# Kernel tuning notes

Hardware: AMD Instinct MI355X
Metric: run time of the kernel (lower is better)

The kernel has to match this reference:

```python
import jax, jax.numpy as jnp
import numpy as np

D_MODEL, NHEAD, DIM_FF = 256, 8, 2048
B, Q, HW = 8, 100, 128 * 128
EPS = 1e-5


def _layernorm(x, g, b):
    mu = jnp.mean(x, axis=-1, keepdims=True)
    var = jnp.mean(jnp.square(x - mu), axis=-1, keepdims=True)
    return (x - mu) * jax.lax.rsqrt(var + EPS) * g + b


def _mha(x_q, x_kv, in_w, in_b, out_w, out_b, nhead, mask=None):
    """torch.nn.MultiheadAttention (batch_first). mask: (B*H,Q,S) bool, True=ATTEND."""
    d = x_q.shape[-1]
    wq, wk, wv = jnp.split(in_w, 3, axis=0)
    bq, bk, bv = jnp.split(in_b, 3)
    q = x_q @ wq.T + bq          # (B,Q,d)
    k = x_kv @ wk.T + bk         # (B,S,d)
    v = x_kv @ wv.T + bv
    Bb, Qq, _ = q.shape
    S = k.shape[1]
    hd = d // nhead
    q = q.reshape(Bb, Qq, nhead, hd).transpose(0, 2, 1, 3)   # (B,H,Q,hd)
    k = k.reshape(Bb, S, nhead, hd).transpose(0, 2, 1, 3)    # (B,H,S,hd)
    v = v.reshape(Bb, S, nhead, hd).transpose(0, 2, 1, 3)
    scores = jnp.einsum('bhqd,bhkd->bhqk', q, k) / jnp.sqrt(jnp.asarray(hd, q.dtype))
    if mask is not None:
        m = mask.reshape(Bb, nhead, Qq, S)
        scores = jnp.where(m, scores, -jnp.inf)
    attn = jax.nn.softmax(scores, axis=-1)
    out = jnp.einsum('bhqk,bhkd->bhqd', attn, v)             # (B,H,Q,hd)
    out = out.transpose(0, 2, 1, 3).reshape(Bb, Qq, d)
    return out @ out_w.T + out_b


def setup_inputs() -> dict:
    key = jax.random.key(0)
    ks = jax.random.split(key, 10)
    s = 0.02
    return {
        'queries': jax.random.normal(ks[0], (B, Q, D_MODEL), jnp.float32),
        'pixel_features': jax.random.normal(ks[1], (B, HW, D_MODEL), jnp.float32),
        'attn_mask': jax.random.randint(ks[2], (B * NHEAD, Q, HW), 0, 2).astype(bool),
        'sa_in_w': jax.random.normal(ks[3], (3 * D_MODEL, D_MODEL), jnp.float32) * s,
        'sa_in_b': jnp.zeros((3 * D_MODEL,), jnp.float32),
        'sa_out_w': jax.random.normal(ks[4], (D_MODEL, D_MODEL), jnp.float32) * s,
        'sa_out_b': jnp.zeros((D_MODEL,), jnp.float32),
        'norm1_g': jnp.ones((D_MODEL,), jnp.float32),
        'norm1_b': jnp.zeros((D_MODEL,), jnp.float32),
        'ca_in_w': jax.random.normal(ks[5], (3 * D_MODEL, D_MODEL), jnp.float32) * s,
        'ca_in_b': jnp.zeros((3 * D_MODEL,), jnp.float32),
        'ca_out_w': jax.random.normal(ks[6], (D_MODEL, D_MODEL), jnp.float32) * s,
        'ca_out_b': jnp.zeros((D_MODEL,), jnp.float32),
        'norm2_g': jnp.ones((D_MODEL,), jnp.float32),
        'norm2_b': jnp.zeros((D_MODEL,), jnp.float32),
        'ff_w1': jax.random.normal(ks[7], (DIM_FF, D_MODEL), jnp.float32) * s,
        'ff_b1': jnp.zeros((DIM_FF,), jnp.float32),
        'ff_w2': jax.random.normal(ks[8], (D_MODEL, DIM_FF), jnp.float32) * s,
        'ff_b2': jnp.zeros((D_MODEL,), jnp.float32),
        'norm3_g': jnp.ones((D_MODEL,), jnp.float32),
        'norm3_b': jnp.zeros((D_MODEL,), jnp.float32),
    }


def reference(queries, pixel_features, attn_mask,
              sa_in_w, sa_in_b, sa_out_w, sa_out_b, norm1_g, norm1_b,
              ca_in_w, ca_in_b, ca_out_w, ca_out_b, norm2_g, norm2_b,
              ff_w1, ff_b1, ff_w2, ff_b2, norm3_g, norm3_b):
    # 1) self-attention among queries (post-norm residual)
    sa = _mha(queries, queries, sa_in_w, sa_in_b, sa_out_w, sa_out_b, NHEAD)
    x = _layernorm(queries + sa, norm1_g, norm1_b)
    # 2) masked cross-attention (attn_mask: True = attend)
    ca = _mha(x, pixel_features, ca_in_w, ca_in_b, ca_out_w, ca_out_b, NHEAD, mask=attn_mask)
    x = _layernorm(x + ca, norm2_g, norm2_b)
    # 3) FFN
    h = jax.nn.relu(x @ ff_w1.T + ff_b1)
    ff = h @ ff_w2.T + ff_b2
    return _layernorm(x + ff, norm3_g, norm3_b)
```

## Files before the change

kernel.cpp:

```cpp
#include <hip/hip_runtime.h>

#define SCALE 0.17677669529663687f

typedef __attribute__((ext_vector_type(8))) short frag8;
typedef __attribute__((ext_vector_type(4))) float facc4;

#define MFMA16(a, b, c) __builtin_amdgcn_mfma_f32_16x16x32_bf16((a), (b), (c), 0, 0, 0)

__device__ __forceinline__ unsigned short f2b(float f) {
  union { float f; unsigned u; } v; v.f = f;
  return (unsigned short)((v.u + 0x7fffu + ((v.u >> 16) & 1u)) >> 16);
}
__device__ __forceinline__ unsigned int pack2(float a, float b) {
  return (unsigned int)f2b(a) | ((unsigned int)f2b(b) << 16);
}
__device__ __forceinline__ void gl_lds16(const void* g, void* l) {
  __builtin_amdgcn_global_load_lds((const __attribute__((address_space(1))) unsigned int*)g,
                                   (__attribute__((address_space(3))) unsigned int*)l, 16, 0, 0);
}

__global__ __launch_bounds__(256) void cvt_weights(const float* __restrict__ s0, const float* __restrict__ s1,
                                                   const float* __restrict__ s2, const float* __restrict__ s3,
                                                   const float* __restrict__ s4, const float* __restrict__ s5,
                                                   unsigned short* __restrict__ dst) {
  int bid = blockIdx.x;
  const float* src; int off;
  if (bid < 96)       { src = s0; off = 0; }
  else if (bid < 128) { src = s1; off = 196608; bid -= 96; }
  else if (bid < 224) { src = s2; off = 262144; bid -= 128; }
  else if (bid < 256) { src = s3; off = 458752; bid -= 224; }
  else if (bid < 512) { src = s4; off = 524288; bid -= 256; }
  else                { src = s5; off = 1048576; bid -= 512; }
  int i = bid * 2048 + threadIdx.x * 8;
  float4 a = *(const float4*)(src + i);
  float4 b = *(const float4*)(src + i + 4);
  uint4 p;
  p.x = pack2(a.x, a.y); p.y = pack2(a.z, a.w);
  p.z = pack2(b.x, b.y); p.w = pack2(b.z, b.w);
  *(uint4*)(dst + off + i) = p;
}

__global__ __launch_bounds__(256) void pack_mask(const unsigned char* __restrict__ mask,
                                                 unsigned int* __restrict__ mp) {
  int idx = blockIdx.x * 256 + threadIdx.x;
  if (idx >= 64 * 112 * 512) return;
  int wi = idx & 511;
  int row = (idx >> 9) % 112;
  int bh = idx / (512 * 112);
  unsigned int wv = 0;
  if (row < 100) {
    const unsigned int* src = (const unsigned int*)(mask + (size_t)(bh * 100 + row) * 16384 + wi * 32);
#pragma unroll
    for (int u = 0; u < 8; ++u) {
      unsigned int nib = (((src[u] & 0x01010101u) * 0x01020408u) >> 24) & 0xFu;
      wv |= nib << (u * 4);
    }
  }
  mp[idx] = wv;
}

template <int RELU, int BIAS>
__global__ __launch_bounds__(256) void mfma_gemm(const float* __restrict__ A,
                                                 const unsigned short* __restrict__ Wb,
                                                 const float* __restrict__ bias,
                                                 float* __restrict__ C,
                                                 int M, int N, int Ktot, int Kchunk) {
  __shared__ unsigned short As[64 * 40];
  __shared__ unsigned short Bs[64 * 32];
  const int t = threadIdx.x;
  const int mb = blockIdx.x, nb = blockIdx.y, zb = blockIdx.z;
  const int w = t >> 6, lane = t & 63, quad = lane >> 4, l16 = lane & 15;
  const int kbeg = zb * Kchunk;
  float* Cz = C + (size_t)zb * M * N;
  facc4 acc[4] = {};
  for (int k0 = kbeg; k0 < kbeg + Kchunk; k0 += 32) {
    {
      int r = t >> 2, c = (t & 3) * 8;
      int gr = mb * 64 + r;
      float4 f0 = {}, f1 = {};
      if (gr < M) {
        const float* src = A + (size_t)gr * Ktot + k0 + c;
        f0 = *(const float4*)src; f1 = *(const float4*)(src + 4);
      }
      uint4 p;
      p.x = pack2(f0.x, f0.y); p.y = pack2(f0.z, f0.w);
      p.z = pack2(f1.x, f1.y); p.w = pack2(f1.z, f1.w);
      *(uint4*)&As[r * 40 + c] = p;
    }
    {
      int row = w * 16 + (lane >> 2);
      gl_lds16(Wb + (size_t)(nb * 64 + row) * Ktot + k0 + (lane & 3) * 8, Bs + w * 512);
    }
    __syncthreads();
    frag8 af = *(const frag8*)(As + (w * 16 + l16) * 40 + quad * 8);
#pragma unroll
    for (int nt = 0; nt < 4; ++nt) {
      frag8 bf = *(const frag8*)(Bs + (nt * 16 + l16) * 32 + quad * 8);
      acc[nt] = MFMA16(af, bf, acc[nt]);
    }
    __syncthreads();
  }
#pragma unroll
  for (int nt = 0; nt < 4; ++nt)
#pragma unroll
    for (int rg = 0; rg < 4; ++rg) {
      int row = mb * 64 + w * 16 + quad * 4 + rg;
      int col = nb * 64 + nt * 16 + l16;
      if (row < M) {
        float v = acc[nt][rg] + (BIAS ? bias[col] : 0.f);
        if (RELU) v = fmaxf(v, 0.f);
        Cz[(size_t)row * N + col] = v;
      }
    }
}

__global__ __launch_bounds__(256) void res_ln(const float* __restrict__ y,
                                              const float* __restrict__ resid,
                                              const float* __restrict__ g,
                                              const float* __restrict__ bv,
                                              float* __restrict__ out) {
  const int r = blockIdx.x, t = threadIdx.x;
  float v = y[(size_t)r * 256 + t] + resid[(size_t)r * 256 + t];
  __shared__ float red[8];
  float s1 = v, s2 = v * v;
#pragma unroll
  for (int off = 1; off < 64; off <<= 1) { s1 += __shfl_xor(s1, off, 64); s2 += __shfl_xor(s2, off, 64); }
  if ((t & 63) == 0) { red[t >> 6] = s1; red[4 + (t >> 6)] = s2; }
  __syncthreads();
  float S1 = red[0] + red[1] + red[2] + red[3];
  float S2 = red[4] + red[5] + red[6] + red[7];
  float mu = S1 * (1.f / 256.f);
  float var = S2 * (1.f / 256.f) - mu * mu;
  float inv = rsqrtf(var + 1e-5f);
  out[(size_t)r * 256 + t] = (v - mu) * inv * g[t] + bv[t];
}

__global__ __launch_bounds__(256) void res_ln4(const float* __restrict__ p,
                                               const float* __restrict__ bias,
                                               const float* __restrict__ resid,
                                               const float* __restrict__ g,
                                               const float* __restrict__ bv,
                                               float* __restrict__ out) {
  const int r = blockIdx.x, t = threadIdx.x;
  size_t i = (size_t)r * 256 + t;
  float v = p[i] + p[i + 204800] + p[i + 409600] + p[i + 614400] + bias[t] + resid[i];
  __shared__ float red[8];
  float s1 = v, s2 = v * v;
#pragma unroll
  for (int off = 1; off < 64; off <<= 1) { s1 += __shfl_xor(s1, off, 64); s2 += __shfl_xor(s2, off, 64); }
  if ((t & 63) == 0) { red[t >> 6] = s1; red[4 + (t >> 6)] = s2; }
  __syncthreads();
  float S1 = red[0] + red[1] + red[2] + red[3];
  float S2 = red[4] + red[5] + red[6] + red[7];
  float mu = S1 * (1.f / 256.f);
  float var = S2 * (1.f / 256.f) - mu * mu;
  float inv = rsqrtf(var + 1e-5f);
  out[i] = (v - mu) * inv * g[t] + bv[t];
}

__global__ __launch_bounds__(256) void self_attn(const float* __restrict__ qkv,
                                                 float* __restrict__ out) {
  const int wid = blockIdx.x * 4 + (threadIdx.x >> 6);
  const int lane = threadIdx.x & 63;
  const int bh = wid / 100, q = wid - bh * 100;
  const int b = bh >> 3, h = bh & 7;
  float4 qv[8];
  {
    const float4* qr = (const float4*)(qkv + (size_t)(b * 100 + q) * 768 + h * 32);
#pragma unroll
    for (int i = 0; i < 8; ++i) {
      float4 x = qr[i];
      qv[i] = make_float4(x.x * SCALE, x.y * SCALE, x.z * SCALE, x.w * SCALE);
    }
  }
  float l = 0.f;
  float4 O[8] = {};
  for (int k0 = 0; k0 < 128; k0 += 64) {
    int k = k0 + lane;
    int kc = (k < 100) ? k : 0;
    const float4* kr = (const float4*)(qkv + (size_t)(b * 100 + kc) * 768 + 256 + h * 32);
    float s = 0.f;
#pragma unroll
    for (int i = 0; i < 8; ++i) {
      float4 kx = kr[i];
      s += qv[i].x * kx.x + qv[i].y * kx.y + qv[i].z * kx.z + qv[i].w * kx.w;
    }
    float p = (k < 100) ? __expf(s) : 0.f;
    l += p;
    const float4* vr = (const float4*)(qkv + (size_t)(b * 100 + kc) * 768 + 512 + h * 32);
#pragma unroll
    for (int i = 0; i < 8; ++i) {
      float4 vx = vr[i];
      O[i].x += p * vx.x; O[i].y += p * vx.y; O[i].z += p * vx.z; O[i].w += p * vx.w;
    }
  }
#pragma unroll
  for (int off = 1; off < 64; off <<= 1) {
    l += __shfl_xor(l, off, 64);
#pragma unroll
    for (int i = 0; i < 8; ++i) {
      O[i].x += __shfl_xor(O[i].x, off, 64);
      O[i].y += __shfl_xor(O[i].y, off, 64);
      O[i].z += __shfl_xor(O[i].z, off, 64);
      O[i].w += __shfl_xor(O[i].w, off, 64);
    }
  }
  if (lane < 32) {
    float inv = 1.f / l;
    int i4 = lane >> 2, sub = lane & 3;
    float ov = 0.f;
#pragma unroll
    for (int i = 0; i < 8; ++i) {
      if (i4 == i) {
        float4 vv = O[i];
        ov = (sub == 0) ? vv.x : (sub == 1) ? vv.y : (sub == 2) ? vv.z : vv.w;
      }
    }
    out[(size_t)(b * 100 + q) * 256 + h * 32 + lane] = ov * inv;
  }
}

__global__ __launch_bounds__(512) void kv_proj(const float* __restrict__ pix,
                                               const unsigned short* __restrict__ wkv,
                                               const float* __restrict__ bkv,
                                               unsigned short* __restrict__ Kbuf,
                                               unsigned short* __restrict__ Vt) {
  __shared__ unsigned short smem[2560 + 16384];
  unsigned short* As = smem;
  unsigned short* Bs = smem + 2560;
  const int t = threadIdx.x;
  const int mb = blockIdx.x;
  const int w = t >> 6, lane = t & 63, quad = lane >> 4, l16 = lane & 15;
  const int b = mb >> 8;
  const int hw0 = (mb & 255) * 64;

  facc4 acc[4][4] = {};
  for (int k0 = 0; k0 < 256; k0 += 32) {
    {
      int r = t >> 3, c = (t & 7) * 4;
      float4 f = *(const float4*)(pix + (size_t)(mb * 64 + r) * 256 + k0 + c);
      uint2 p; p.x = pack2(f.x, f.y); p.y = pack2(f.z, f.w);
      *(uint2*)&As[r * 40 + c] = p;
    }
    {
#pragma unroll
      for (int i = 0; i < 4; ++i) {
        int seg = w * 4 + i;
        int row = seg * 16 + (lane >> 2);
        gl_lds16(wkv + (size_t)row * 256 + k0 + (lane & 3) * 8, Bs + seg * 512);
      }
    }
    __syncthreads();
    frag8 af[4], bf[4];
#pragma unroll
    for (int mt = 0; mt < 4; ++mt) af[mt] = *(const frag8*)(As + (mt * 16 + l16) * 40 + quad * 8);
#pragma unroll
    for (int nt = 0; nt < 4; ++nt) bf[nt] = *(const frag8*)(Bs + (w * 64 + nt * 16 + l16) * 32 + quad * 8);
#pragma unroll
    for (int mt = 0; mt < 4; ++mt)
#pragma unroll
      for (int nt = 0; nt < 4; ++nt) acc[mt][nt] = MFMA16(af[mt], bf[nt], acc[mt][nt]);
    __syncthreads();
  }
  {
    unsigned short* Cs = smem;
    if (w < 4) {
#pragma unroll
      for (int mt = 0; mt < 4; ++mt)
#pragma unroll
        for (int nt = 0; nt < 4; ++nt) {
          int col = w * 64 + nt * 16 + l16;
          float bvv = bkv[col];
#pragma unroll
          for (int rg = 0; rg < 4; ++rg)
            Cs[(mt * 16 + quad * 4 + rg) * 264 + col] = f2b(acc[mt][nt][rg] + bvv);
        }
    }
    __syncthreads();
    int key = t >> 3, h = t & 7;
    const unsigned short* src = &Cs[key * 264 + h * 32];
    unsigned short* dst = Kbuf + ((size_t)((b * 8 + h) * 16384 + hw0 + key)) * 32;
    uint4 c0 = *(const uint4*)src, c1 = *(const uint4*)(src + 8);
    uint4 c2 = *(const uint4*)(src + 16), c3 = *(const uint4*)(src + 24);
    *(uint4*)dst = c0; *(uint4*)(dst + 8) = c1; *(uint4*)(dst + 16) = c2; *(uint4*)(dst + 24) = c3;
  }
  __syncthreads();
  {
    unsigned short* Cst = smem;
    if (w >= 4) {
#pragma unroll
      for (int mt = 0; mt < 4; ++mt)
#pragma unroll
        for (int nt = 0; nt < 4; ++nt) {
          int colv = (w - 4) * 64 + nt * 16 + l16;
          float bvv = bkv[256 + colv];
#pragma unroll
          for (int rg = 0; rg < 4; ++rg)
            Cst[colv * 72 + (mt * 16 + quad * 4 + rg)] = f2b(acc[mt][nt][rg] + bvv);
        }
    }
    __syncthreads();
    int dr = t >> 1, half = t & 1;
    const unsigned short* src = &Cst[dr * 72 + half * 32];
    unsigned short* dst = Vt + ((size_t)(b * 8 + (dr >> 5)) * 32 + (dr & 31)) * 16384 + hw0 + half * 32;
    uint4 c0 = *(const uint4*)src, c1 = *(const uint4*)(src + 8);
    uint4 c2 = *(const uint4*)(src + 16), c3 = *(const uint4*)(src + 24);
    *(uint4*)dst = c0; *(uint4*)(dst + 8) = c1; *(uint4*)(dst + 16) = c2; *(uint4*)(dst + 24) = c3;
  }
}

__global__ __launch_bounds__(256) void cross_attn(const float* __restrict__ qc,
                                                  const unsigned short* __restrict__ Kbuf,
                                                  const unsigned short* __restrict__ Vt,
                                                  const unsigned int* __restrict__ maskp,
                                                  float* __restrict__ Opart,
                                                  float* __restrict__ lpart) {
  const int bh = blockIdx.x >> 3;
  const int chunk = blockIdx.x & 7;
  const int b = bh >> 3, h = bh & 7;
  const int t = threadIdx.x;
  const int w = t >> 6, lane = t & 63, quad = lane >> 4, l16 = lane & 15;

  __shared__ unsigned short Qs[112 * 40];
  for (int i = t; i < 112 * 32; i += 256) {
    int r = i >> 5, d = i & 31;
    float v = (r < 100) ? qc[(size_t)(b * 100 + r) * 256 + h * 32 + d] * SCALE : 0.f;
    Qs[r * 40 + d] = f2b(v);
  }
  __syncthreads();

  frag8 qf[7];
#pragma unroll
  for (int qt = 0; qt < 7; ++qt) qf[qt] = *(const frag8*)(Qs + (qt * 16 + l16) * 40 + quad * 8);

  facc4 o[7][2] = {};
  float lacc[7] = {};
  const facc4 zacc = {0.f, 0.f, 0.f, 0.f};
  const int keybase = chunk * 2048 + w * 512;
  const unsigned short* Kb = Kbuf + (size_t)bh * 16384 * 32;
  const unsigned short* Vb = Vt + (size_t)bh * 32 * 16384;
  const unsigned int* mrow = maskp + (size_t)bh * 112 * 512;

  for (int it = 0; it < 16; ++it) {
    const int kk = keybase + it * 32;
    frag8 kf0 = *(const frag8*)(Kb + (size_t)(kk + l16) * 32 + quad * 8);
    frag8 kf1 = *(const frag8*)(Kb + (size_t)(kk + 16 + l16) * 32 + quad * 8);
    frag8 vf[2];
#pragma unroll
    for (int dt = 0; dt < 2; ++dt) {
      const unsigned short* vp = Vb + (size_t)(dt * 16 + l16) * 16384 + kk + quad * 4;
      ushort4 lo = *(const ushort4*)vp;
      ushort4 hi = *(const ushort4*)(vp + 16);
      frag8 v;
      v[0] = (short)lo.x; v[1] = (short)lo.y; v[2] = (short)lo.z; v[3] = (short)lo.w;
      v[4] = (short)hi.x; v[5] = (short)hi.y; v[6] = (short)hi.z; v[7] = (short)hi.w;
      vf[dt] = v;
    }
    const int wi = kk >> 5;
#pragma unroll
    for (int qt = 0; qt < 7; ++qt) {
      facc4 s0 = MFMA16(kf0, qf[qt], zacc);
      facc4 s1 = MFMA16(kf1, qf[qt], zacc);
      unsigned int mw = mrow[(qt * 16 + l16) * 512 + wi];
      float p[8];
#pragma unroll
      for (int rg = 0; rg < 4; ++rg) {
        float e0 = __expf(s0[rg]);
        float e1 = __expf(s1[rg]);
        p[rg]     = ((mw >> (quad * 4 + rg)) & 1u) ? e0 : 0.f;
        p[4 + rg] = ((mw >> (16 + quad * 4 + rg)) & 1u) ? e1 : 0.f;
      }
      lacc[qt] += p[0] + p[1] + p[2] + p[3] + p[4] + p[5] + p[6] + p[7];
      frag8 pa;
#pragma unroll
      for (int j = 0; j < 8; ++j) pa[j] = (short)f2b(p[j]);
      o[qt][0] = MFMA16(pa, vf[0], o[qt][0]);
      o[qt][1] = MFMA16(pa, vf[1], o[qt][1]);
    }
  }
#pragma unroll
  for (int qt = 0; qt < 7; ++qt) {
    lacc[qt] += __shfl_xor(lacc[qt], 16, 64);
    lacc[qt] += __shfl_xor(lacc[qt], 32, 64);
  }
  const int pidx = chunk * 4 + w;
  float* Op = Opart + ((size_t)bh * 32 + pidx) * 112 * 32;
  float* lp = lpart + ((size_t)bh * 32 + pidx) * 112;
#pragma unroll
  for (int qt = 0; qt < 7; ++qt) {
#pragma unroll
    for (int rg = 0; rg < 4; ++rg) {
      int row = qt * 16 + quad * 4 + rg;
      Op[row * 32 + l16] = o[qt][0][rg];
      Op[row * 32 + 16 + l16] = o[qt][1][rg];
    }
    if (lane < 16) lp[qt * 16 + lane] = lacc[qt];
  }
}

__global__ __launch_bounds__(256) void cross_combine(const float* __restrict__ Opart,
                                                     const float* __restrict__ lpart,
                                                     float* __restrict__ out) {
  const int bid = blockIdx.x;
  const int bh = bid / 13, qg = bid - bh * 13;
  const int t = threadIdx.x;
  const int q = qg * 8 + (t >> 5), d = t & 31;
  if (q >= 100) return;
  const int b = bh >> 3, h = bh & 7;
  float osum = 0.f, lsum = 0.f;
#pragma unroll 4
  for (int p = 0; p < 32; ++p) {
    osum += Opart[(((size_t)bh * 32 + p) * 112 + q) * 32 + d];
    lsum += lpart[((size_t)bh * 32 + p) * 112 + q];
  }
  out[(size_t)(b * 100 + q) * 256 + h * 32 + d] = osum / lsum;
}

extern "C" void kernel_launch(void* const* d_in, const int* in_sizes, int n_in,
                              void* d_out, int out_size, void* d_ws, size_t ws_size,
                              hipStream_t stream) {
  const float* queries = (const float*)d_in[0];
  const float* pix = (const float*)d_in[1];
  const unsigned char* mask = (const unsigned char*)d_in[2];
  const float* sa_in_w = (const float*)d_in[3];
  const float* sa_in_b = (const float*)d_in[4];
  const float* sa_out_w = (const float*)d_in[5];
  const float* sa_out_b = (const float*)d_in[6];
  const float* n1g = (const float*)d_in[7];
  const float* n1b = (const float*)d_in[8];
  const float* ca_in_w = (const float*)d_in[9];
  const float* ca_in_b = (const float*)d_in[10];
  const float* ca_out_w = (const float*)d_in[11];
  const float* ca_out_b = (const float*)d_in[12];
  const float* n2g = (const float*)d_in[13];
  const float* n2b = (const float*)d_in[14];
  const float* ff_w1 = (const float*)d_in[15];
  const float* ff_b1 = (const float*)d_in[16];
  const float* ff_w2 = (const float*)d_in[17];
  const float* ff_b2 = (const float*)d_in[18];
  const float* n3g = (const float*)d_in[19];
  const float* n3b = (const float*)d_in[20];
  float* out = (float*)d_out;
  char* ws = (char*)d_ws;

  unsigned short* Kbuf = (unsigned short*)(ws + 0);
  unsigned short* Vt   = (unsigned short*)(ws + 67108864);
  unsigned short* wb   = (unsigned short*)(ws + 134217728);
  unsigned int* maskp  = (unsigned int*)(ws + 137363456);
  float* qkvs   = (float*)(ws + 152043520);
  float* sao    = (float*)(ws + 154501120);
  float* ptmp   = (float*)(ws + 155320320);
  float* x1     = (float*)(ws + 158597120);
  float* qc     = (float*)(ws + 159416320);
  float* Opart  = (float*)(ws + 160235520);
  float* lpart  = (float*)(ws + 189595648);
  float* ca_out = (float*)(ws + 190513152);
  float* x2     = (float*)(ws + 191332352);
  float* hffn   = (float*)(ws + 192151552);

  const unsigned short* wb_sain  = wb;
  const unsigned short* wb_saout = wb + 196608;
  const unsigned short* wb_caq   = wb + 262144;
  const unsigned short* wb_cakv  = wb + 327680;
  const unsigned short* wb_caout = wb + 458752;
  const unsigned short* wb_ff1   = wb + 524288;
  const unsigned short* wb_ff2   = wb + 1048576;

  cvt_weights<<<768, 256, 0, stream>>>(sa_in_w, sa_out_w, ca_in_w, ca_out_w, ff_w1, ff_w2, wb);
  pack_mask<<<14336, 256, 0, stream>>>(mask, maskp);

  mfma_gemm<0, 1><<<dim3(13, 12, 1), 256, 0, stream>>>(queries, wb_sain, sa_in_b, qkvs, 800, 768, 256, 256);
  self_attn<<<1600, 256, 0, stream>>>(qkvs, sao);
  mfma_gemm<0, 1><<<dim3(13, 4, 1), 256, 0, stream>>>(sao, wb_saout, sa_out_b, ptmp, 800, 256, 256, 256);
  res_ln<<<800, 256, 0, stream>>>(ptmp, queries, n1g, n1b, x1);

  mfma_gemm<0, 1><<<dim3(13, 4, 1), 256, 0, stream>>>(x1, wb_caq, ca_in_b, qc, 800, 256, 256, 256);
  kv_proj<<<2048, 512, 0, stream>>>(pix, wb_cakv, ca_in_b + 256, Kbuf, Vt);
  cross_attn<<<512, 256, 0, stream>>>(qc, Kbuf, Vt, maskp, Opart, lpart);
  cross_combine<<<64 * 13, 256, 0, stream>>>(Opart, lpart, ca_out);
  mfma_gemm<0, 1><<<dim3(13, 4, 1), 256, 0, stream>>>(ca_out, wb_caout, ca_out_b, ptmp, 800, 256, 256, 256);
  res_ln<<<800, 256, 0, stream>>>(ptmp, x1, n2g, n2b, x2);

  mfma_gemm<1, 1><<<dim3(13, 32, 1), 256, 0, stream>>>(x2, wb_ff1, ff_b1, hffn, 800, 2048, 256, 256);
  mfma_gemm<0, 0><<<dim3(13, 4, 4), 256, 0, stream>>>(hffn, wb_ff2, nullptr, ptmp, 800, 256, 2048, 512);
  res_ln4<<<800, 256, 0, stream>>>(ptmp, ff_b2, x2, n3g, n3b, out);
}
```

Measured before the change: 867.1 us.

## Fuse K/V projection, mask packing and cross-attention into one kernel

Replaces the separate kv_proj, pack_mask and cross_attn kernels with a single ca_fused kernel. It projects each 32-key pixel tile to per-head K and V on the fly with MFMA, reads the raw byte mask directly, and uses exp2 with a folded log2e scale. This avoids writing and re-reading 128MB of bf16 K/V and the packed mask. Partial outputs are stored as bf16 and pixels are truncated rather than rounded to bf16. The cost is that every head recomputes projections from a shared pixel tile, weight fragments are reread from global memory in the inner loop, and the grid is only 256 blocks, which may underfill the GPU.

```diff
diff --git a/kernel.cpp b/kernel.cpp
--- a/kernel.cpp
+++ b/kernel.cpp
@@ -1,6 +1,7 @@
 #include <hip/hip_runtime.h>
 
 #define SCALE 0.17677669529663687f
+#define SCALE2 (0.17677669529663687f * 1.4426950408889634f)
 
 typedef __attribute__((ext_vector_type(8))) short frag8;
 typedef __attribute__((ext_vector_type(4))) float facc4;
@@ -11,13 +12,23 @@
   union { float f; unsigned u; } v; v.f = f;
   return (unsigned short)((v.u + 0x7fffu + ((v.u >> 16) & 1u)) >> 16);
 }
+__device__ __forceinline__ float b2f(unsigned short h) {
+  union { unsigned u; float f; } v; v.u = ((unsigned)h) << 16;
+  return v.f;
+}
 __device__ __forceinline__ unsigned int pack2(float a, float b) {
   return (unsigned int)f2b(a) | ((unsigned int)f2b(b) << 16);
+}
+__device__ __forceinline__ unsigned int tpack(float a, float b) {
+  union { float f; unsigned u; } x, y; x.f = a; y.f = b;
+  return (x.u >> 16) | (y.u & 0xffff0000u);
 }
 __device__ __forceinline__ void gl_lds16(const void* g, void* l) {
   __builtin_amdgcn_global_load_lds((const __attribute__((address_space(1))) unsigned int*)g,
                                    (__attribute__((address_space(3))) unsigned int*)l, 16, 0, 0);
 }
+
+union F8U { frag8 f; unsigned u[4]; };
 
 __global__ __launch_bounds__(256) void cvt_weights(const float* __restrict__ s0, const float* __restrict__ s1,
                                                    const float* __restrict__ s2, const float* __restrict__ s3,
@@ -38,25 +49,6 @@
   p.x = pack2(a.x, a.y); p.y = pack2(a.z, a.w);
   p.z = pack2(b.x, b.y); p.w = pack2(b.z, b.w);
   *(uint4*)(dst + off + i) = p;
-}
-
-__global__ __launch_bounds__(256) void pack_mask(const unsigned char* __restrict__ mask,
-                                                 unsigned int* __restrict__ mp) {
-  int idx = blockIdx.x * 256 + threadIdx.x;
-  if (idx >= 64 * 112 * 512) return;
-  int wi = idx & 511;
-  int row = (idx >> 9) % 112;
-  int bh = idx / (512 * 112);
-  unsigned int wv = 0;
-  if (row < 100) {
-    const unsigned int* src = (const unsigned int*)(mask + (size_t)(bh * 100 + row) * 16384 + wi * 32);
-#pragma unroll
-    for (int u = 0; u < 8; ++u) {
-      unsigned int nib = (((src[u] & 0x01010101u) * 0x01020408u) >> 24) & 0xFu;
-      wv |= nib << (u * 4);
-    }
-  }
-  mp[idx] = wv;
 }
 
 template <int RELU, int BIAS>
@@ -220,185 +212,152 @@
   }
 }
 
-__global__ __launch_bounds__(512) void kv_proj(const float* __restrict__ pix,
-                                               const unsigned short* __restrict__ wkv,
-                                               const float* __restrict__ bkv,
-                                               unsigned short* __restrict__ Kbuf,
-                                               unsigned short* __restrict__ Vt) {
-  __shared__ unsigned short smem[2560 + 16384];
-  unsigned short* As = smem;
-  unsigned short* Bs = smem + 2560;
+__global__ __launch_bounds__(512, 2) void ca_fused(const float* __restrict__ qc,
+                                                   const unsigned short* __restrict__ wkv,
+                                                   const float* __restrict__ bkv,
+                                                   const float* __restrict__ pix,
+                                                   const unsigned char* __restrict__ mask,
+                                                   unsigned short* __restrict__ Opartb,
+                                                   float* __restrict__ lpart) {
+  const int bid = blockIdx.x;
+  const int b = bid >> 5, chunk = bid & 31;
   const int t = threadIdx.x;
-  const int mb = blockIdx.x;
-  const int w = t >> 6, lane = t & 63, quad = lane >> 4, l16 = lane & 15;
-  const int b = mb >> 8;
-  const int hw0 = (mb & 255) * 64;
-
-  facc4 acc[4][4] = {};
-  for (int k0 = 0; k0 < 256; k0 += 32) {
-    {
-      int r = t >> 3, c = (t & 7) * 4;
-      float4 f = *(const float4*)(pix + (size_t)(mb * 64 + r) * 256 + k0 + c);
-      uint2 p; p.x = pack2(f.x, f.y); p.y = pack2(f.z, f.w);
-      *(uint2*)&As[r * 40 + c] = p;
-    }
-    {
-#pragma unroll
-      for (int i = 0; i < 4; ++i) {
-        int seg = w * 4 + i;
-        int row = seg * 16 + (lane >> 2);
-        gl_lds16(wkv + (size_t)row * 256 + k0 + (lane & 3) * 8, Bs + seg * 512);
-      }
-    }
-    __syncthreads();
-    frag8 af[4], bf[4];
-#pragma unroll
-    for (int mt = 0; mt < 4; ++mt) af[mt] = *(const frag8*)(As + (mt * 16 + l16) * 40 + quad * 8);
-#pragma unroll
-    for (int nt = 0; nt < 4; ++nt) bf[nt] = *(const frag8*)(Bs + (w * 64 + nt * 16 + l16) * 32 + quad * 8);
-#pragma unroll
-    for (int mt = 0; mt < 4; ++mt)
-#pragma unroll
-      for (int nt = 0; nt < 4; ++nt) acc[mt][nt] = MFMA16(af[mt], bf[nt], acc[mt][nt]);
-    __syncthreads();
-  }
-  {
-    unsigned short* Cs = smem;
-    if (w < 4) {
-#pragma unroll
-      for (int mt = 0; mt < 4; ++mt)
-#pragma unroll
-        for (int nt = 0; nt < 4; ++nt) {
-          int col = w * 64 + nt * 16 + l16;
-          float bvv = bkv[col];
-#pragma unroll
-          for (int rg = 0; rg < 4; ++rg)
-            Cs[(mt * 16 + quad * 4 + rg) * 264 + col] = f2b(acc[mt][nt][rg] + bvv);
-        }
-    }
-    __syncthreads();
-    int key = t >> 3, h = t & 7;
-    const unsigned short* src = &Cs[key * 264 + h * 32];
-    unsigned short* dst = Kbuf + ((size_t)((b * 8 + h) * 16384 + hw0 + key)) * 32;
-    uint4 c0 = *(const uint4*)src, c1 = *(const uint4*)(src + 8);
-    uint4 c2 = *(const uint4*)(src + 16), c3 = *(const uint4*)(src + 24);
-    *(uint4*)dst = c0; *(uint4*)(dst + 8) = c1; *(uint4*)(dst + 16) = c2; *(uint4*)(dst + 24) = c3;
-  }
-  __syncthreads();
-  {
-    unsigned short* Cst = smem;
-    if (w >= 4) {
-#pragma unroll
-      for (int mt = 0; mt < 4; ++mt)
-#pragma unroll
-        for (int nt = 0; nt < 4; ++nt) {
-          int colv = (w - 4) * 64 + nt * 16 + l16;
-          float bvv = bkv[256 + colv];
-#pragma unroll
-          for (int rg = 0; rg < 4; ++rg)
-            Cst[colv * 72 + (mt * 16 + quad * 4 + rg)] = f2b(acc[mt][nt][rg] + bvv);
-        }
-    }
-    __syncthreads();
-    int dr = t >> 1, half = t & 1;
-    const unsigned short* src = &Cst[dr * 72 + half * 32];
-    unsigned short* dst = Vt + ((size_t)(b * 8 + (dr >> 5)) * 32 + (dr & 31)) * 16384 + hw0 + half * 32;
-    uint4 c0 = *(const uint4*)src, c1 = *(const uint4*)(src + 8);
-    uint4 c2 = *(const uint4*)(src + 16), c3 = *(const uint4*)(src + 24);
-    *(uint4*)dst = c0; *(uint4*)(dst + 8) = c1; *(uint4*)(dst + 16) = c2; *(uint4*)(dst + 24) = c3;
-  }
-}
-
-__global__ __launch_bounds__(256) void cross_attn(const float* __restrict__ qc,
-                                                  const unsigned short* __restrict__ Kbuf,
-                                                  const unsigned short* __restrict__ Vt,
-                                                  const unsigned int* __restrict__ maskp,
-                                                  float* __restrict__ Opart,
-                                                  float* __restrict__ lpart) {
-  const int bh = blockIdx.x >> 3;
-  const int chunk = blockIdx.x & 7;
-  const int b = bh >> 3, h = bh & 7;
-  const int t = threadIdx.x;
-  const int w = t >> 6, lane = t & 63, quad = lane >> 4, l16 = lane & 15;
-
-  __shared__ unsigned short Qs[112 * 40];
-  for (int i = t; i < 112 * 32; i += 256) {
-    int r = i >> 5, d = i & 31;
-    float v = (r < 100) ? qc[(size_t)(b * 100 + r) * 256 + h * 32 + d] * SCALE : 0.f;
-    Qs[r * 40 + d] = f2b(v);
-  }
-  __syncthreads();
+  const int h = t >> 6, lane = t & 63, quad = lane >> 4, l16 = lane & 15;
+  const int bh = b * 8 + h;
+
+  __shared__ unsigned short PixS[8 * 32 * 40];
 
   frag8 qf[7];
 #pragma unroll
-  for (int qt = 0; qt < 7; ++qt) qf[qt] = *(const frag8*)(Qs + (qt * 16 + l16) * 40 + quad * 8);
+  for (int qt = 0; qt < 7; ++qt) {
+    int r = qt * 16 + l16;
+    float4 f0 = {}, f1 = {};
+    if (r < 100) {
+      const float* qrow = qc + (size_t)(b * 100 + r) * 256 + h * 32 + quad * 4;
+      f0 = *(const float4*)qrow;
+      f1 = *(const float4*)(qrow + 16);
+    }
+    F8U u;
+    u.u[0] = pack2(f0.x * SCALE2, f0.y * SCALE2);
+    u.u[1] = pack2(f0.z * SCALE2, f0.w * SCALE2);
+    u.u[2] = pack2(f1.x * SCALE2, f1.y * SCALE2);
+    u.u[3] = pack2(f1.z * SCALE2, f1.w * SCALE2);
+    qf[qt] = u.f;
+  }
+
+  float bK[2][4], bV[2];
+#pragma unroll
+  for (int mf = 0; mf < 2; ++mf) {
+#pragma unroll
+    for (int rg = 0; rg < 4; ++rg) bK[mf][rg] = bkv[h * 32 + mf * 16 + quad * 4 + rg];
+    bV[mf] = bkv[256 + h * 32 + mf * 16 + l16];
+  }
+
+  const unsigned short* wkbase = wkv + (size_t)(h * 32) * 256;
+  const unsigned short* wvbase = wkv + (size_t)(256 + h * 32) * 256;
 
   facc4 o[7][2] = {};
   float lacc[7] = {};
   const facc4 zacc = {0.f, 0.f, 0.f, 0.f};
-  const int keybase = chunk * 2048 + w * 512;
-  const unsigned short* Kb = Kbuf + (size_t)bh * 16384 * 32;
-  const unsigned short* Vb = Vt + (size_t)bh * 32 * 16384;
-  const unsigned int* mrow = maskp + (size_t)bh * 112 * 512;
 
   for (int it = 0; it < 16; ++it) {
-    const int kk = keybase + it * 32;
-    frag8 kf0 = *(const frag8*)(Kb + (size_t)(kk + l16) * 32 + quad * 8);
-    frag8 kf1 = *(const frag8*)(Kb + (size_t)(kk + 16 + l16) * 32 + quad * 8);
-    frag8 vf[2];
-#pragma unroll
-    for (int dt = 0; dt < 2; ++dt) {
-      const unsigned short* vp = Vb + (size_t)(dt * 16 + l16) * 16384 + kk + quad * 4;
-      ushort4 lo = *(const ushort4*)vp;
-      ushort4 hi = *(const ushort4*)(vp + 16);
-      frag8 v;
-      v[0] = (short)lo.x; v[1] = (short)lo.y; v[2] = (short)lo.z; v[3] = (short)lo.w;
-      v[4] = (short)hi.x; v[5] = (short)hi.y; v[6] = (short)hi.z; v[7] = (short)hi.w;
-      vf[dt] = v;
-    }
-    const int wi = kk >> 5;
+    const int kk = it * 32;
+    const int gkey = chunk * 512 + kk;
+    __syncthreads();
+    {
+      int row = t >> 4, cg = (t & 15) * 16;
+      const float* src = pix + ((size_t)(b * 16384 + gkey + row)) * 256 + cg;
+      float4 a0 = *(const float4*)src;
+      float4 a1 = *(const float4*)(src + 4);
+      float4 a2 = *(const float4*)(src + 8);
+      float4 a3 = *(const float4*)(src + 12);
+      uint4 u0, u1;
+      u0.x = tpack(a0.x, a0.y); u0.y = tpack(a0.z, a0.w);
+      u0.z = tpack(a1.x, a1.y); u0.w = tpack(a1.z, a1.w);
+      u1.x = tpack(a2.x, a2.y); u1.y = tpack(a2.z, a2.w);
+      u1.z = tpack(a3.x, a3.y); u1.w = tpack(a3.z, a3.w);
+      unsigned short* d = PixS + (cg >> 5) * 1280 + row * 40 + (cg & 31);
+      *(uint4*)d = u0; *(uint4*)(d + 8) = u1;
+    }
+    __syncthreads();
+
+    facc4 ka[2][2] = {}, va[2][2] = {};
+#pragma unroll
+    for (int cb = 0; cb < 8; ++cb) {
+      frag8 pf0 = *(const frag8*)(PixS + cb * 1280 + l16 * 40 + quad * 8);
+      frag8 pf1 = *(const frag8*)(PixS + cb * 1280 + (16 + l16) * 40 + quad * 8);
+      int co = cb * 32 + quad * 8;
+      frag8 wk0 = *(const frag8*)(wkbase + (size_t)l16 * 256 + co);
+      frag8 wk1 = *(const frag8*)(wkbase + (size_t)(16 + l16) * 256 + co);
+      frag8 wv0 = *(const frag8*)(wvbase + (size_t)l16 * 256 + co);
+      frag8 wv1 = *(const frag8*)(wvbase + (size_t)(16 + l16) * 256 + co);
+      ka[0][0] = MFMA16(wk0, pf0, ka[0][0]); ka[0][1] = MFMA16(wk0, pf1, ka[0][1]);
+      ka[1][0] = MFMA16(wk1, pf0, ka[1][0]); ka[1][1] = MFMA16(wk1, pf1, ka[1][1]);
+      va[0][0] = MFMA16(pf0, wv0, va[0][0]); va[0][1] = MFMA16(pf0, wv1, va[0][1]);
+      va[1][0] = MFMA16(pf1, wv0, va[1][0]); va[1][1] = MFMA16(pf1, wv1, va[1][1]);
+    }
+    frag8 kfA0, kfA1, vfB0, vfB1;
+    {
+      F8U k0u, k1u, v0u, v1u;
+#pragma unroll
+      for (int pr = 0; pr < 4; ++pr) {
+        int mf = pr >> 1, r0 = (pr & 1) * 2, r1 = r0 + 1;
+        k0u.u[pr] = tpack(ka[mf][0][r0] + bK[mf][r0], ka[mf][0][r1] + bK[mf][r1]);
+        k1u.u[pr] = tpack(ka[mf][1][r0] + bK[mf][r0], ka[mf][1][r1] + bK[mf][r1]);
+        v0u.u[pr] = tpack(va[mf][0][r0] + bV[0], va[mf][0][r1] + bV[0]);
+        v1u.u[pr] = tpack(va[mf][1][r0] + bV[1], va[mf][1][r1] + bV[1]);
+      }
+      kfA0 = k0u.f; kfA1 = k1u.f; vfB0 = v0u.f; vfB1 = v1u.f;
+    }
+
+    const unsigned char* mbase = mask + (size_t)bh * 100 * 16384 + gkey + quad * 4;
 #pragma unroll
     for (int qt = 0; qt < 7; ++qt) {
-      facc4 s0 = MFMA16(kf0, qf[qt], zacc);
-      facc4 s1 = MFMA16(kf1, qf[qt], zacc);
-      unsigned int mw = mrow[(qt * 16 + l16) * 512 + wi];
+      facc4 s0 = MFMA16(kfA0, qf[qt], zacc);
+      facc4 s1 = MFMA16(kfA1, qf[qt], zacc);
+      int r = qt * 16 + l16;
+      int rc = (r < 100) ? r : 99;
+      const unsigned char* mrow = mbase + (size_t)rc * 16384;
+      unsigned m0 = *(const unsigned*)mrow;
+      unsigned m1 = *(const unsigned*)(mrow + 16);
+      if (r >= 100) { m0 = 0; m1 = 0; }
       float p[8];
 #pragma unroll
       for (int rg = 0; rg < 4; ++rg) {
-        float e0 = __expf(s0[rg]);
-        float e1 = __expf(s1[rg]);
-        p[rg]     = ((mw >> (quad * 4 + rg)) & 1u) ? e0 : 0.f;
-        p[4 + rg] = ((mw >> (16 + quad * 4 + rg)) & 1u) ? e1 : 0.f;
+        float e0 = exp2f(s0[rg]);
+        float e1 = exp2f(s1[rg]);
+        p[rg] = ((m0 >> (rg * 8)) & 1u) ? e0 : 0.f;
+        p[4 + rg] = ((m1 >> (rg * 8)) & 1u) ? e1 : 0.f;
       }
       lacc[qt] += p[0] + p[1] + p[2] + p[3] + p[4] + p[5] + p[6] + p[7];
-      frag8 pa;
-#pragma unroll
-      for (int j = 0; j < 8; ++j) pa[j] = (short)f2b(p[j]);
-      o[qt][0] = MFMA16(pa, vf[0], o[qt][0]);
-      o[qt][1] = MFMA16(pa, vf[1], o[qt][1]);
-    }
-  }
+      F8U pu;
+      pu.u[0] = tpack(p[0], p[1]); pu.u[1] = tpack(p[2], p[3]);
+      pu.u[2] = tpack(p[4], p[5]); pu.u[3] = tpack(p[6], p[7]);
+      o[qt][0] = MFMA16(pu.f, vfB0, o[qt][0]);
+      o[qt][1] = MFMA16(pu.f, vfB1, o[qt][1]);
+    }
+  }
+
 #pragma unroll
   for (int qt = 0; qt < 7; ++qt) {
     lacc[qt] += __shfl_xor(lacc[qt], 16, 64);
     lacc[qt] += __shfl_xor(lacc[qt], 32, 64);
   }
-  const int pidx = chunk * 4 + w;
-  float* Op = Opart + ((size_t)bh * 32 + pidx) * 112 * 32;
-  float* lp = lpart + ((size_t)bh * 32 + pidx) * 112;
+  unsigned short* Op = Opartb + ((size_t)bh * 32 + chunk) * 112 * 32;
+  float* lp = lpart + ((size_t)bh * 32 + chunk) * 112;
 #pragma unroll
   for (int qt = 0; qt < 7; ++qt) {
 #pragma unroll
     for (int rg = 0; rg < 4; ++rg) {
       int row = qt * 16 + quad * 4 + rg;
-      Op[row * 32 + l16] = o[qt][0][rg];
-      Op[row * 32 + 16 + l16] = o[qt][1][rg];
+      Op[row * 32 + l16] = f2b(o[qt][0][rg]);
+      Op[row * 32 + 16 + l16] = f2b(o[qt][1][rg]);
     }
     if (lane < 16) lp[qt * 16 + lane] = lacc[qt];
   }
 }
 
-__global__ __launch_bounds__(256) void cross_combine(const float* __restrict__ Opart,
+__global__ __launch_bounds__(256) void cross_combine(const unsigned short* __restrict__ Opartb,
                                                      const float* __restrict__ lpart,
                                                      float* __restrict__ out) {
   const int bid = blockIdx.x;
@@ -410,7 +369,7 @@
   float osum = 0.f, lsum = 0.f;
 #pragma unroll 4
   for (int p = 0; p < 32; ++p) {
-    osum += Opart[(((size_t)bh * 32 + p) * 112 + q) * 32 + d];
+    osum += b2f(Opartb[(((size_t)bh * 32 + p) * 112 + q) * 32 + d]);
     lsum += lpart[((size_t)bh * 32 + p) * 112 + q];
   }
   out[(size_t)(b * 100 + q) * 256 + h * 32 + d] = osum / lsum;
@@ -443,16 +402,13 @@
   float* out = (float*)d_out;
   char* ws = (char*)d_ws;
 
-  unsigned short* Kbuf = (unsigned short*)(ws + 0);
-  unsigned short* Vt   = (unsigned short*)(ws + 67108864);
   unsigned short* wb   = (unsigned short*)(ws + 134217728);
-  unsigned int* maskp  = (unsigned int*)(ws + 137363456);
   float* qkvs   = (float*)(ws + 152043520);
   float* sao    = (float*)(ws + 154501120);
   float* ptmp   = (float*)(ws + 155320320);
   float* x1     = (float*)(ws + 158597120);
   float* qc     = (float*)(ws + 159416320);
-  float* Opart  = (float*)(ws + 160235520);
+  unsigned short* Opartb = (unsigned short*)(ws + 160235520);
   float* lpart  = (float*)(ws + 189595648);
   float* ca_out = (float*)(ws + 190513152);
   float* x2     = (float*)(ws + 191332352);
@@ -467,7 +423,6 @@
   const unsigned short* wb_ff2   = wb + 1048576;
 
   cvt_weights<<<768, 256, 0, stream>>>(sa_in_w, sa_out_w, ca_in_w, ca_out_w, ff_w1, ff_w2, wb);
-  pack_mask<<<14336, 256, 0, stream>>>(mask, maskp);
 
   mfma_gemm<0, 1><<<dim3(13, 12, 1), 256, 0, stream>>>(queries, wb_sain, sa_in_b, qkvs, 800, 768, 256, 256);
   self_attn<<<1600, 256, 0, stream>>>(qkvs, sao);
@@ -475,9 +430,8 @@
   res_ln<<<800, 256, 0, stream>>>(ptmp, queries, n1g, n1b, x1);
 
   mfma_gemm<0, 1><<<dim3(13, 4, 1), 256, 0, stream>>>(x1, wb_caq, ca_in_b, qc, 800, 256, 256, 256);
-  kv_proj<<<2048, 512, 0, stream>>>(pix, wb_cakv, ca_in_b + 256, Kbuf, Vt);
-  cross_attn<<<512, 256, 0, stream>>>(qc, Kbuf, Vt, maskp, Opart, lpart);
-  cross_combine<<<64 * 13, 256, 0, stream>>>(Opart, lpart, ca_out);
+  ca_fused<<<256, 512, 0, stream>>>(qc, wb_cakv, ca_in_b + 256, pix, mask, Opartb, lpart);
+  cross_combine<<<64 * 13, 256, 0, stream>>>(Opartb, lpart, ca_out);
   mfma_gemm<0, 1><<<dim3(13, 4, 1), 256, 0, stream>>>(ca_out, wb_caout, ca_out_b, ptmp, 800, 256, 256, 256);
   res_ln<<<800, 256, 0, stream>>>(ptmp, x1, n2g, n2b, x2);
 
```

Result: faster. 807.7 us (-6.9%).
